# Optimization experiments

Hardware: AMD Instinct MI355X
Metric: run time of the kernel (lower is better)

The kernel has to match this reference:

```python
import jax, jax.numpy as jnp
import numpy as np

THRESHOLD = 0.5
TEMPERATURE = 4.0
LOG_CLAMP = -100.0  # matches torch BCELoss log clamping


def setup_inputs() -> dict:
    key = jax.random.key(0)
    k1, k2, k3, k4 = jax.random.split(key, 4)
    B, C = 8192, 4096
    output = jax.random.uniform(k1, (B, C), dtype=jnp.float32)
    output_consistency = jax.random.uniform(k2, (B, C), dtype=jnp.float32)
    label = jax.random.uniform(k3, (B, C), dtype=jnp.float32)
    source = jax.random.randint(k4, (B,), 0, 2, dtype=jnp.int64)
    return {"output": output, "output_consistency": output_consistency,
            "label": label, "source": source}


def reference(output, output_consistency, label, source):
    B = output.shape[0]
    # per-element BCE (nn.BCELoss default reduction='mean' on a scalar = the scalar loss)
    log_p = jnp.maximum(jnp.log(output), LOG_CLAMP)
    log_1mp = jnp.maximum(jnp.log1p(-output), LOG_CLAMP)
    bce = -(label * log_p + (1.0 - label) * log_1mp)  # [B,C]
    # BCE only accumulated when source[b] in {0, 1}
    src_mask = ((source == 0) | (source == 1)).astype(output.dtype)[:, None]  # [B,1]
    bce_sum = jnp.sum(bce * src_mask)
    # conditional sharpening
    sharp = jnp.where(output > THRESHOLD,
                      output + (1.0 - output) / TEMPERATURE,
                      output - output / TEMPERATURE)
    pseudo_loss = jnp.sum((output - sharp) ** 2)
    consistency_loss = jnp.sum((output_consistency - sharp) ** 2)
    return (bce_sum + consistency_loss + pseudo_loss) / B
```

## Files before the change

### kernel.cpp

```cpp
#include <hip/hip_runtime.h>

#define B_DIM 8192
#define C_DIM 4096
#define NBLOCKS 2048
#define NTHREADS 256

#define LOG2_CLAMP (-144.26950408889634f)
#define LN2 0.6931471805599453f

__global__ __launch_bounds__(NTHREADS) void semiloss_partial_kernel(
        const float* __restrict__ out,
        const float* __restrict__ cons,
        const float* __restrict__ lab,
        const int* __restrict__ source,
        float* __restrict__ partial)
{
    const unsigned n4 = (unsigned)(B_DIM) * (unsigned)(C_DIM) / 4u;
    unsigned tid    = blockIdx.x * (unsigned)blockDim.x + threadIdx.x;
    unsigned stride = gridDim.x * (unsigned)blockDim.x;

    const float4* __restrict__ o4 = (const float4*)out;
    const float4* __restrict__ c4 = (const float4*)cons;
    const float4* __restrict__ l4 = (const float4*)lab;

    float acc_b  = 0.0f;
    float acc_u2 = 0.0f;
    float acc_d2 = 0.0f;

    for (unsigned i = tid; i < n4; i += stride) {
        float4 o  = o4[i];
        float4 oc = c4[i];

        {
            float s0 = (o.x > 0.5f) ? 1.0f : 0.0f;
            float u  = o.x - s0;
            float sh = fmaf(-0.25f, u, o.x);
            float d2 = oc.x - sh;
            acc_u2 = fmaf(u, u, acc_u2);
            acc_d2 = fmaf(d2, d2, acc_d2);
        }
        {
            float s0 = (o.y > 0.5f) ? 1.0f : 0.0f;
            float u  = o.y - s0;
            float sh = fmaf(-0.25f, u, o.y);
            float d2 = oc.y - sh;
            acc_u2 = fmaf(u, u, acc_u2);
            acc_d2 = fmaf(d2, d2, acc_d2);
        }
        {
            float s0 = (o.z > 0.5f) ? 1.0f : 0.0f;
            float u  = o.z - s0;
            float sh = fmaf(-0.25f, u, o.z);
            float d2 = oc.z - sh;
            acc_u2 = fmaf(u, u, acc_u2);
            acc_d2 = fmaf(d2, d2, acc_d2);
        }
        {
            float s0 = (o.w > 0.5f) ? 1.0f : 0.0f;
            float u  = o.w - s0;
            float sh = fmaf(-0.25f, u, o.w);
            float d2 = oc.w - sh;
            acc_u2 = fmaf(u, u, acc_u2);
            acc_d2 = fmaf(d2, d2, acc_d2);
        }

        unsigned row = i >> 10;
        int s = source[row];
        if ((unsigned)s <= 1u) {
            float4 l = l4[i];
            {
                float lp = fmaxf(__log2f(o.x), LOG2_CLAMP);
                float lq = fmaxf(__log2f(1.0f - o.x), LOG2_CLAMP);
                acc_b = fmaf(l.x, lp - lq, acc_b + lq);
            }
            {
                float lp = fmaxf(__log2f(o.y), LOG2_CLAMP);
                float lq = fmaxf(__log2f(1.0f - o.y), LOG2_CLAMP);
                acc_b = fmaf(l.y, lp - lq, acc_b + lq);
            }
            {
                float lp = fmaxf(__log2f(o.z), LOG2_CLAMP);
                float lq = fmaxf(__log2f(1.0f - o.z), LOG2_CLAMP);
                acc_b = fmaf(l.z, lp - lq, acc_b + lq);
            }
            {
                float lp = fmaxf(__log2f(o.w), LOG2_CLAMP);
                float lq = fmaxf(__log2f(1.0f - o.w), LOG2_CLAMP);
                acc_b = fmaf(l.w, lp - lq, acc_b + lq);
            }
        }
    }

    float acc = fmaf(-LN2, acc_b, fmaf(0.0625f, acc_u2, acc_d2));

    #pragma unroll
    for (int off = 32; off > 0; off >>= 1)
        acc += __shfl_down(acc, off, 64);

    __shared__ float red[NTHREADS / 64];
    int lane = threadIdx.x & 63;
    int wave = threadIdx.x >> 6;
    if (lane == 0) red[wave] = acc;
    __syncthreads();

    if (threadIdx.x == 0) {
        float s = 0.0f;
        #pragma unroll
        for (int w = 0; w < NTHREADS / 64; ++w) s += red[w];
        partial[blockIdx.x] = s;
    }
}

__global__ __launch_bounds__(NTHREADS) void semiloss_final_kernel(
        const float* __restrict__ partial, float* __restrict__ dout)
{
    float acc = 0.0f;
    for (int i = threadIdx.x; i < NBLOCKS; i += NTHREADS)
        acc += partial[i];

    #pragma unroll
    for (int off = 32; off > 0; off >>= 1)
        acc += __shfl_down(acc, off, 64);

    __shared__ float red[NTHREADS / 64];
    int lane = threadIdx.x & 63;
    int wave = threadIdx.x >> 6;
    if (lane == 0) red[wave] = acc;
    __syncthreads();

    if (threadIdx.x == 0) {
        float s = 0.0f;
        #pragma unroll
        for (int w = 0; w < NTHREADS / 64; ++w) s += red[w];
        dout[0] = s / (float)B_DIM;
    }
}

extern "C" void kernel_launch(void* const* d_in, const int* in_sizes, int n_in,
                              void* d_out, int out_size, void* d_ws, size_t ws_size,
                              hipStream_t stream) {
    const float* out  = (const float*)d_in[0];
    const float* cons = (const float*)d_in[1];
    const float* lab  = (const float*)d_in[2];
    const int*   src  = (const int*)d_in[3];

    float* partial = (float*)d_ws;
    float* dout    = (float*)d_out;

    semiloss_partial_kernel<<<NBLOCKS, NTHREADS, 0, stream>>>(out, cons, lab, src, partial);
    semiloss_final_kernel<<<1, NTHREADS, 0, stream>>>(partial, dout);
}
```

Before: 74.65 us.

## Fully unroll grid-stride loop with register prefetch and precomputed source mask

Replaces the dynamic grid-stride loop with a fixed 16-iteration unrolled loop that prefetches the next float4 of all three inputs while computing the current one. Source values for every row the thread visits are loaded up front into a bitmask. The label is now always loaded and the BCE is always computed, then multiplied by the mask, so the branch and its divergence go away. The aim is more memory-level parallelism in exchange for more registers and unconditional label traffic. Rows whose source is outside {0,1} now still pay for the label read.

```diff
diff --git a/kernel.cpp b/kernel.cpp
--- a/kernel.cpp
+++ b/kernel.cpp
@@ -4,9 +4,44 @@
 #define C_DIM 4096
 #define NBLOCKS 2048
 #define NTHREADS 256
+#define NITER 16
 
 #define LOG2_CLAMP (-144.26950408889634f)
 #define LN2 0.6931471805599453f
+
+__device__ __forceinline__ void sq_terms(float o, float oc, float& acc_u2, float& acc_d2) {
+    float s0 = (o > 0.5f) ? 1.0f : 0.0f;
+    float u  = o - s0;
+    float sh = fmaf(-0.25f, u, o);
+    float d2 = oc - sh;
+    acc_u2 = fmaf(u, u, acc_u2);
+    acc_d2 = fmaf(d2, d2, acc_d2);
+}
+
+__device__ __forceinline__ float bce_group(float4 o, float4 l) {
+    float bb = 0.0f;
+    {
+        float lp = fmaxf(__log2f(o.x), LOG2_CLAMP);
+        float lq = fmaxf(__log2f(1.0f - o.x), LOG2_CLAMP);
+        bb = fmaf(l.x, lp - lq, bb + lq);
+    }
+    {
+        float lp = fmaxf(__log2f(o.y), LOG2_CLAMP);
+        float lq = fmaxf(__log2f(1.0f - o.y), LOG2_CLAMP);
+        bb = fmaf(l.y, lp - lq, bb + lq);
+    }
+    {
+        float lp = fmaxf(__log2f(o.z), LOG2_CLAMP);
+        float lq = fmaxf(__log2f(1.0f - o.z), LOG2_CLAMP);
+        bb = fmaf(l.z, lp - lq, bb + lq);
+    }
+    {
+        float lp = fmaxf(__log2f(o.w), LOG2_CLAMP);
+        float lq = fmaxf(__log2f(1.0f - o.w), LOG2_CLAMP);
+        bb = fmaf(l.w, lp - lq, bb + lq);
+    }
+    return bb;
+}
 
 __global__ __launch_bounds__(NTHREADS) void semiloss_partial_kernel(
         const float* __restrict__ out,
@@ -15,80 +50,48 @@
         const int* __restrict__ source,
         float* __restrict__ partial)
 {
-    const unsigned n4 = (unsigned)(B_DIM) * (unsigned)(C_DIM) / 4u;
-    unsigned tid    = blockIdx.x * (unsigned)blockDim.x + threadIdx.x;
-    unsigned stride = gridDim.x * (unsigned)blockDim.x;
+    const unsigned stride = NBLOCKS * NTHREADS;
+    const unsigned tid = blockIdx.x * (unsigned)NTHREADS + threadIdx.x;
 
     const float4* __restrict__ o4 = (const float4*)out;
     const float4* __restrict__ c4 = (const float4*)cons;
     const float4* __restrict__ l4 = (const float4*)lab;
 
+    unsigned row0 = tid >> 10;
+    unsigned bits = 0;
+    #pragma unroll
+    for (int k = 0; k < NITER; ++k) {
+        int s = source[row0 + (unsigned)k * (stride >> 10)];
+        bits |= (((unsigned)s <= 1u) ? 1u : 0u) << k;
+    }
+
     float acc_b  = 0.0f;
     float acc_u2 = 0.0f;
     float acc_d2 = 0.0f;
 
-    for (unsigned i = tid; i < n4; i += stride) {
-        float4 o  = o4[i];
-        float4 oc = c4[i];
+    float4 o = o4[tid];
+    float4 c = c4[tid];
+    float4 l = l4[tid];
 
-        {
-            float s0 = (o.x > 0.5f) ? 1.0f : 0.0f;
-            float u  = o.x - s0;
-            float sh = fmaf(-0.25f, u, o.x);
-            float d2 = oc.x - sh;
-            acc_u2 = fmaf(u, u, acc_u2);
-            acc_d2 = fmaf(d2, d2, acc_d2);
-        }
-        {
-            float s0 = (o.y > 0.5f) ? 1.0f : 0.0f;
-            float u  = o.y - s0;
-            float sh = fmaf(-0.25f, u, o.y);
-            float d2 = oc.y - sh;
-            acc_u2 = fmaf(u, u, acc_u2);
-            acc_d2 = fmaf(d2, d2, acc_d2);
-        }
-        {
-            float s0 = (o.z > 0.5f) ? 1.0f : 0.0f;
-            float u  = o.z - s0;
-            float sh = fmaf(-0.25f, u, o.z);
-            float d2 = oc.z - sh;
-            acc_u2 = fmaf(u, u, acc_u2);
-            acc_d2 = fmaf(d2, d2, acc_d2);
-        }
-        {
-            float s0 = (o.w > 0.5f) ? 1.0f : 0.0f;
-            float u  = o.w - s0;
-            float sh = fmaf(-0.25f, u, o.w);
-            float d2 = oc.w - sh;
-            acc_u2 = fmaf(u, u, acc_u2);
-            acc_d2 = fmaf(d2, d2, acc_d2);
+    #pragma unroll
+    for (int k = 0; k < NITER; ++k) {
+        float4 on, cn, ln;
+        if (k < NITER - 1) {
+            unsigned inext = tid + (unsigned)(k + 1) * stride;
+            on = o4[inext];
+            cn = c4[inext];
+            ln = l4[inext];
         }
 
-        unsigned row = i >> 10;
-        int s = source[row];
-        if ((unsigned)s <= 1u) {
-            float4 l = l4[i];
-            {
-                float lp = fmaxf(__log2f(o.x), LOG2_CLAMP);
-                float lq = fmaxf(__log2f(1.0f - o.x), LOG2_CLAMP);
-                acc_b = fmaf(l.x, lp - lq, acc_b + lq);
-            }
-            {
-                float lp = fmaxf(__log2f(o.y), LOG2_CLAMP);
-                float lq = fmaxf(__log2f(1.0f - o.y), LOG2_CLAMP);
-                acc_b = fmaf(l.y, lp - lq, acc_b + lq);
-            }
-            {
-                float lp = fmaxf(__log2f(o.z), LOG2_CLAMP);
-                float lq = fmaxf(__log2f(1.0f - o.z), LOG2_CLAMP);
-                acc_b = fmaf(l.z, lp - lq, acc_b + lq);
-            }
-            {
-                float lp = fmaxf(__log2f(o.w), LOG2_CLAMP);
-                float lq = fmaxf(__log2f(1.0f - o.w), LOG2_CLAMP);
-                acc_b = fmaf(l.w, lp - lq, acc_b + lq);
-            }
-        }
+        float m = (bits & (1u << k)) ? 1.0f : 0.0f;
+
+        sq_terms(o.x, c.x, acc_u2, acc_d2);
+        sq_terms(o.y, c.y, acc_u2, acc_d2);
+        sq_terms(o.z, c.z, acc_u2, acc_d2);
+        sq_terms(o.w, c.w, acc_u2, acc_d2);
+        acc_b = fmaf(m, bce_group(o, l), acc_b);
+
+        if (k < NITER - 1) { o = on; c = cn; l = ln; }
     }
 
     float acc = fmaf(-LN2, acc_b, fmaf(0.0625f, acc_u2, acc_d2));
```

Result: slower. 78.27 us (+4.9%).
